# Kernel optimization log

Measured on AMD Instinct MI355X. Metric: run time of the kernel, lower is better.

The kernel has to match this reference:

```python
import jax, jax.numpy as jnp
import numpy as np

HEADS = 16
HEAD_DIM = 64


def _attn(q, k, v):
    # q: [..., Q, h, d], k/v: [..., K, h, d]  (non-causal SDPA, scale 1/sqrt(d))
    scale = 1.0 / np.sqrt(HEAD_DIM).astype(np.float32)
    s = jnp.einsum('...qhd,...khd->...hqk', q, k) * scale
    p = jax.nn.softmax(s, axis=-1)
    return jnp.einsum('...hqk,...khd->...qhd', p, v)


def setup_inputs() -> dict:
    key = jax.random.key(0)
    k0, k1, k2 = jax.random.split(key, 3)
    B, T, H, W, D = 4, 32, 16, 16, 1024
    inner = HEADS * HEAD_DIM
    x = jax.random.normal(k0, (B, T, H, W, D), jnp.float32)
    Wqkv = jax.random.normal(k1, (D, 3 * inner), jnp.float32) / np.sqrt(D)
    Wout = jax.random.normal(k2, (inner, D), jnp.float32) / np.sqrt(inner)
    bout = jnp.zeros((D,), jnp.float32)
    return {"x": x, "Wqkv": Wqkv, "Wout": Wout, "bout": bout, "reference_length": 3}


def reference(x, Wqkv, Wout, bout, reference_length):
    B, T, H, W, D = x.shape
    length = reference_length + 1
    n = T // length            # n_frames (chunks)
    S = H * W                  # tokens per frame
    h, d = HEADS, HEAD_DIM

    qkv = jnp.einsum('bthwD,De->bthwe', x, Wqkv)
    q, k, v = jnp.split(qkv, 3, axis=-1)

    def rs(t):  # -> [B, n, length, S, h, d]
        return t.reshape(B, n, length, S, h, d)

    qr, kr, vr = rs(q), rs(k), rs(v)

    # non-last chunks: query = first frame of chunk, keys/values = remaining r frames
    q_pre = qr[:, :-1, 0]                                             # [B, n-1, S, h, d]
    k_pre = kr[:, :-1, 1:].reshape(B, n - 1, reference_length * S, h, d)
    v_pre = vr[:, :-1, 1:].reshape(B, n - 1, reference_length * S, h, d)
    o_pre = _attn(q_pre, k_pre, v_pre).reshape(B, n - 1, H, W, h * d)

    # last chunk: all `length` frames are queries, keys/values = frames 1..length-1
    q_last = qr[:, -1].reshape(B, length * S, h, d)
    k_last = kr[:, -1, 1:].reshape(B, reference_length * S, h, d)
    v_last = vr[:, -1, 1:].reshape(B, reference_length * S, h, d)
    o_last = _attn(q_last, k_last, v_last).reshape(B, length, H, W, h * d)

    o = jnp.concatenate([o_pre, o_last], axis=1)  # [B, n-1+length, H, W, inner]
    return jnp.einsum('bthwe,eD->bthwD', o, Wout) + bout
```

## Files before the change

### kernel.cpp

```cpp
#include <hip/hip_runtime.h>
#include <hip/hip_bf16.h>

typedef __bf16 bf16;
typedef __bf16 bf16x8 __attribute__((ext_vector_type(8)));
typedef float  f32x4  __attribute__((ext_vector_type(4)));
typedef float  f32x4v __attribute__((ext_vector_type(4)));
typedef unsigned int u32x4 __attribute__((ext_vector_type(4)));
typedef unsigned short u16x4 __attribute__((ext_vector_type(4)));

#define DEV __device__ __forceinline__

DEV void gload_lds16(const bf16* g, bf16* l) {
    __builtin_amdgcn_global_load_lds(
        (__attribute__((address_space(1))) void*)g,
        (__attribute__((address_space(3))) void*)l, 16, 0, 0);
}

DEV bf16x8 as_bf(u32x4 v) { return __builtin_bit_cast(bf16x8, v); }

DEV f32x4 mfma16(bf16x8 a, bf16x8 b, f32x4 c) {
    return __builtin_amdgcn_mfma_f32_16x16x32_bf16(a, b, c, 0, 0, 0);
}

DEV int cvtpk(float lo, float hi) {
    int r;
    asm("v_cvt_pk_bf16_f32 %0, %1, %2" : "=v"(r) : "v"(lo), "v"(hi));
    return r;
}

constexpr int D_   = 1024;
constexpr int S_   = 256;
constexpr int TOUT = 11;
constexpr int MQ   = 4 * TOUT * S_;
constexpr int MKV  = 4 * 8 * 3 * S_;
constexpr int KVL  = 768;

constexpr int PB_WQKV = 768;
constexpr int PB_WOUT = 256;
constexpr int PB_GQ   = MQ  * 128 / 256;
constexpr int PB_GKV  = MKV * 128 / 256;
constexpr int PB_TOT  = PB_WQKV + PB_WOUT + PB_GQ + PB_GKV;

__global__ void prep(const float* __restrict__ x,
                     const float* __restrict__ Wqkv,
                     const float* __restrict__ Wout,
                     bf16* __restrict__ Aq, bf16* __restrict__ Akv,
                     bf16* __restrict__ Wqkv_t, bf16* __restrict__ Wout_t)
{
    __shared__ float T[64][65];
    const int tid = threadIdx.x;
    int wg = blockIdx.x;

    if (wg < PB_WQKV + PB_WOUT) {
        const float* W; bf16* Wt; int N, bid2;
        if (wg < PB_WQKV) { W = Wqkv; Wt = Wqkv_t; N = 3072; bid2 = wg; }
        else              { W = Wout; Wt = Wout_t; N = 1024; bid2 = wg - PB_WQKV; }
        const int kt = bid2 & 15, nt = bid2 >> 4;
        const int k0 = kt * 64, n0 = nt * 64;
        for (int i = 0; i < 16; ++i) {
            const int e = i * 256 + tid;
            const int kk = e >> 6, nn = e & 63;
            T[nn][kk] = W[(size_t)(k0 + kk) * N + n0 + nn];
        }
        __syncthreads();
        for (int i = 0; i < 16; ++i) {
            const int e = i * 256 + tid;
            const int n = e >> 6, kk = e & 63;
            Wt[(size_t)(n0 + n) * 1024 + k0 + kk] = (bf16)T[n][kk];
        }
        return;
    }
    wg -= PB_WQKV + PB_WOUT;

    int row, part;
    const float* src;
    bf16* dst;
    if (wg < PB_GQ) {
        const int idx = wg * 256 + tid;
        row = idx >> 7; part = idx & 127;
        const int b    = row / (TOUT * S_);
        const int r2   = row - b * (TOUT * S_);
        const int tout = r2 >> 8;
        const int s    = r2 & 255;
        const int tx   = tout < 7 ? tout * 4 : 28 + (tout - 7);
        src = x + ((size_t)((b * 32 + tx) * S_ + s)) * D_ + part * 8;
        dst = Aq + (size_t)row * D_ + part * 8;
    } else {
        const int idx = (wg - PB_GQ) * 256 + tid;
        row = idx >> 7; part = idx & 127;
        const int b  = row / 6144;
        const int r2 = row - b * 6144;
        const int c  = r2 / KVL;
        const int j  = r2 - c * KVL;
        const int f  = 1 + (j >> 8);
        const int s  = j & 255;
        const int tx = c * 4 + f;
        src = x + ((size_t)((b * 32 + tx) * S_ + s)) * D_ + part * 8;
        dst = Akv + (size_t)row * D_ + part * 8;
    }
    f32x4v v0 = *(const f32x4v*)src;
    f32x4v v1 = *(const f32x4v*)(src + 4);
    bf16x8 o;
    o[0]=(bf16)v0[0]; o[1]=(bf16)v0[1]; o[2]=(bf16)v0[2]; o[3]=(bf16)v0[3];
    o[4]=(bf16)v1[0]; o[5]=(bf16)v1[1]; o[6]=(bf16)v1[2]; o[7]=(bf16)v1[3];
    *(bf16x8*)dst = o;
}

#define PH_BEGIN() do { \
    __builtin_amdgcn_s_barrier(); \
    asm volatile("s_waitcnt lgkmcnt(0)" ::: "memory"); \
    __builtin_amdgcn_sched_barrier(0); \
    __builtin_amdgcn_s_setprio(1); \
} while(0)

#define PH_MMEND() do { \
    __builtin_amdgcn_s_setprio(0); \
    __builtin_amdgcn_sched_barrier(0); \
} while(0)

#define PH_CLOSE() do { \
    asm volatile("s_waitcnt vmcnt(6)" ::: "memory"); \
    __builtin_amdgcn_s_barrier(); \
} while(0)

#define STAGE_A(bufc, half, tile) do { \
    const bf16* s0_ = pA + (size_t)(half) * 64 * 1024 + (tile) * 64; \
    bf16* d0_ = ldsA + (bufc) * 16384 + (half) * 8192; \
    gload_lds16(s0_, d0_); \
    gload_lds16(s0_ + (size_t)128 * 1024, d0_ + 4096); \
} while(0)

#define STAGE_B(bufc, half, tile) do { \
    const bf16* s0_ = pB + (size_t)(half) * 32 * 1024 + (tile) * 64; \
    bf16* d0_ = ldsB + (bufc) * 16384 + (half) * 8192; \
    gload_lds16(s0_, d0_); \
    gload_lds16(s0_ + (size_t)128 * 1024, d0_ + 4096); \
} while(0)

#define LDAJ(dst, bufc, mh, J) do { \
    const bf16* p_ = sm + (bufc) * 16384 + (mh) * 8192 + (J) * 1024; \
    dst[J][0] = *(const u32x4*)(p_ + eA0); \
    dst[J][1] = *(const u32x4*)(p_ + eA1); \
} while(0)

#define LDBH(dst, bufc, nh) do { \
    const bf16* p_ = sm + 32768 + (bufc) * 16384 + (nh) * 8192; \
    dst[0][0] = *(const u32x4*)(p_ + eB0); \
    dst[0][1] = *(const u32x4*)(p_ + eB1); \
    dst[1][0] = *(const u32x4*)(p_ + 1024 + eB0); \
    dst[1][1] = *(const u32x4*)(p_ + 1024 + eB1); \
} while(0)

#define MMX(av, bv, mh, nh) do { \
    _Pragma("unroll") \
    for (int j_ = 0; j_ < 4; ++j_) { \
        _Pragma("unroll") \
        for (int i_ = 0; i_ < 2; ++i_) { \
            f32x4 c_ = acc[(mh)*4 + j_][(nh)*2 + i_]; \
            c_ = mfma16(as_bf(av[j_][0]), as_bf(bv[i_][0]), c_); \
            c_ = mfma16(as_bf(av[j_][1]), as_bf(bv[i_][1]), c_); \
            acc[(mh)*4 + j_][(nh)*2 + i_] = c_; \
        } \
    } \
} while(0)

#define GEMM_MAINLOOP() do { \
    STAGE_A(0, 0, 0); STAGE_A(0, 1, 0); STAGE_B(0, 0, 0); STAGE_B(0, 1, 0); \
    STAGE_A(1, 0, 1); STAGE_B(1, 0, 1); STAGE_B(1, 1, 1); \
    asm volatile("s_waitcnt vmcnt(6)" ::: "memory"); \
    __builtin_amdgcn_s_barrier(); \
    LDAJ(aX,0,0,0); LDAJ(aX,0,0,1); LDAJ(aX,0,0,2); LDAJ(aX,0,0,3); \
    LDBH(bP,0,0); \
    _Pragma("unroll 1") \
    for (int t = 0; t < 8; ++t) { \
        const int T1 = 2 * t + 1; \
        const int n0 = (2 * t + 2 < 15) ? 2 * t + 2 : 15; \
        const int n1 = (2 * t + 3 < 15) ? 2 * t + 3 : 15; \
        STAGE_A(1, 1, T1); \
        PH_BEGIN(); MMX(aX, bP, 0, 0); PH_MMEND(); \
        LDBH(bQ, 0, 1); LDAJ(aY, 0, 1, 0); \
        PH_CLOSE(); \
        STAGE_A(0, 0, n0); \
        PH_BEGIN(); MMX(aX, bQ, 0, 1); PH_MMEND(); \
        LDAJ(aY, 0, 1, 1); LDAJ(aY, 0, 1, 2); LDAJ(aY, 0, 1, 3); \
        PH_CLOSE(); \
        STAGE_B(0, 0, n0); \
        PH_BEGIN(); MMX(aY, bP, 1, 0); PH_MMEND(); \
        LDAJ(aX, 1, 0, 0); LDAJ(aX, 1, 0, 1); LDAJ(aX, 1, 0, 2); \
        PH_CLOSE(); \
        STAGE_B(0, 1, n0); \
        PH_BEGIN(); MMX(aY, bQ, 1, 1); PH_MMEND(); \
        LDAJ(aX, 1, 0, 3); LDBH(bP, 1, 0); \
        PH_CLOSE(); \
        STAGE_A(0, 1, n0); \
        PH_BEGIN(); MMX(aX, bP, 0, 0); PH_MMEND(); \
        LDBH(bQ, 1, 1); LDAJ(aY, 1, 1, 0); \
        PH_CLOSE(); \
        STAGE_A(1, 0, n1); \
        PH_BEGIN(); MMX(aX, bQ, 0, 1); PH_MMEND(); \
        LDAJ(aY, 1, 1, 1); LDAJ(aY, 1, 1, 2); LDAJ(aY, 1, 1, 3); \
        PH_CLOSE(); \
        STAGE_B(1, 0, n1); \
        PH_BEGIN(); MMX(aY, bP, 1, 0); PH_MMEND(); \
        LDAJ(aX, 0, 0, 0); LDAJ(aX, 0, 0, 1); LDAJ(aX, 0, 0, 2); \
        PH_CLOSE(); \
        STAGE_B(1, 1, n1); \
        PH_BEGIN(); MMX(aY, bQ, 1, 1); PH_MMEND(); \
        LDAJ(aX, 0, 0, 3); LDBH(bP, 0, 0); \
        PH_CLOSE(); \
    } \
    asm volatile("s_waitcnt vmcnt(0) lgkmcnt(0)" ::: "memory"); \
} while(0)

#define GEMM_PREAMBLE() \
    const int wr = wid >> 2, wc = wid & 3; \
    const int l15 = lane & 15, l4 = lane >> 4; \
    const int Rrow = (wid << 3) + (lane >> 3); \
    const int G    = (lane & 7) ^ (lane >> 3); \
    const bf16* pA = A  + (size_t)(bm * 256 + Rrow) * 1024 + G * 8; \
    const int wc1 = Rrow >> 5, cc1 = Rrow & 31; \
    const bf16* pB = Bt + (size_t)(bn * 256 + wc1 * 64 + cc1) * 1024 + G * 8; \
    bf16* ldsA = sm + (wid << 9); \
    bf16* ldsB = sm + 32768 + (wid << 9); \
    const int g0  = l4 ^ (l15 & 7); \
    const int eA0 = wr * 4096 + l15 * 64 + g0 * 8; \
    const int eA1 = eA0 ^ 32; \
    const int eB0 = wc * 2048 + l15 * 64 + g0 * 8; \
    const int eB1 = eB0 ^ 32; \
    f32x4 acc[8][4]; \
    u32x4 aX[4][2], aY[4][2], bP[2][2], bQ[2][2]; \
    { const f32x4 zf_ = {0.f, 0.f, 0.f, 0.f}; \
      _Pragma("unroll") \
      for (int m_ = 0; m_ < 8; ++m_) \
          _Pragma("unroll") \
          for (int n_ = 0; n_ < 4; ++n_) acc[m_][n_] = zf_; }

__global__ __launch_bounds__(512, 2) void gemm_qkv(
    const bf16* __restrict__ Aq, const bf16* __restrict__ Akv,
    const bf16* __restrict__ Wt,
    bf16* __restrict__ Qb, bf16* __restrict__ Kb, bf16* __restrict__ Vt)
{
    __shared__ bf16 sm[65536];
    const int tid = threadIdx.x, lane = tid & 63, wid = tid >> 6;

    int wg = blockIdx.x;
    {
        const int xcd = wg & 7, off = wg >> 3;
        wg = xcd * 118 + off;
    }
    const bool isQ = wg < 176;
    const bf16* A;  const bf16* Bt;  int bm, bn;
    if (isQ) {
        const int sg = wg >> 4, s = wg & 15;
        bm = sg * 4 + (s >> 2);
        bn = s & 3;
        A = Aq;  Bt = Wt;
    } else {
        const int id2 = wg - 176;
        const int sg = id2 >> 4, s = id2 & 15;
        bm = (sg % 24) * 4 + (s >> 2);
        bn = (sg / 24) * 4 + (s & 3);
        A = Akv; Bt = Wt + (size_t)1024 * 1024;
    }

    GEMM_PREAMBLE();
    GEMM_MAINLOOP();

    if (isQ || bn < 4) {
        bf16* C = isQ ? Qb : Kb;
        #pragma unroll
        for (int m = 0; m < 8; ++m) {
            const int row = bm * 256 + wr * 128 + m * 16 + l4 * 4;
            #pragma unroll
            for (int n = 0; n < 4; ++n) {
                const int col = bn * 256 + wc * 64 + n * 16 + l15;
                f32x4 v = acc[m][n];
                #pragma unroll
                for (int r = 0; r < 4; ++r)
                    C[(size_t)(row + r) * 1024 + col] = (bf16)v[r];
            }
        }
    } else {
        const int vb = bm / 3;
        const int j0base = (bm % 3) * 256;
        #pragma unroll
        for (int m = 0; m < 8; ++m) {
            const int j0 = j0base + wr * 128 + m * 16 + l4 * 4;
            #pragma unroll
            for (int n = 0; n < 4; ++n) {
                const int colv = (bn - 4) * 256 + wc * 64 + n * 16 + l15;
                f32x4 v = acc[m][n];
                u16x4 pk;
                #pragma unroll
                for (int r = 0; r < 4; ++r) {
                    bf16 t = (bf16)v[r];
                    pk[r] = __builtin_bit_cast(unsigned short, t);
                }
                *(u16x4*)(Vt + ((size_t)vb * 1024 + colv) * KVL + j0) = pk;
            }
        }
    }
}

__global__ __launch_bounds__(512, 2) void gemm_out(
    const bf16* __restrict__ A, const bf16* __restrict__ Bt,
    float* __restrict__ Cf, const float* __restrict__ bias)
{
    __shared__ bf16 sm[65536];
    const int tid = threadIdx.x, lane = tid & 63, wid = tid >> 6;

    int wg = blockIdx.x;
    {
        const int xcd = wg & 7, off = wg >> 3;
        wg = xcd * 22 + off;
    }
    const int sg = wg >> 4, s = wg & 15;
    const int bm = sg * 4 + (s >> 2), bn = s & 3;

    GEMM_PREAMBLE();
    GEMM_MAINLOOP();

    #pragma unroll
    for (int m = 0; m < 8; ++m) {
        const int row = bm * 256 + wr * 128 + m * 16 + l4 * 4;
        #pragma unroll
        for (int n = 0; n < 4; ++n) {
            const int col = bn * 256 + wc * 64 + n * 16 + l15;
            f32x4 v = acc[m][n];
            const float bs = bias[col];
            #pragma unroll
            for (int r = 0; r < 4; ++r)
                Cf[(size_t)(row + r) * 1024 + col] = v[r] + bs;
        }
    }
}

__global__ __launch_bounds__(256, 4) void attn_fwd(
    const bf16* __restrict__ Q, const bf16* __restrict__ K,
    const bf16* __restrict__ Vt, bf16* __restrict__ O)
{
    __shared__ bf16 Kl[2][2][64][32];
    __shared__ bf16 Vl[2][2][64][32];

    const int tid = threadIdx.x, lane = tid & 63, wid = tid >> 6;
    int bid = blockIdx.x;
    const int h = bid & 15; bid >>= 4;
    const int qt = bid % 44, b = bid / 44;
    const int chunk = qt < 28 ? (qt >> 2) : 7;
    const int qrow0 = b * (TOUT * S_) +
                      (qt < 28 ? chunk * S_ + (qt & 3) * 64 : 7 * S_ + (qt - 28) * 64);

    const bf16* kg = K  + ((size_t)(b * 8 + chunk) * KVL) * 1024 + h * 64;
    const bf16* vg = Vt + ((size_t)((b * 8 + chunk) * 16 + h)) * 64 * KVL;

    const int l15 = lane & 15, l4 = lane >> 4;

    const bf16* qp = Q + (size_t)(qrow0 + wid * 16 + l15) * D_ + h * 64 + l4 * 8;
    u32x4 q0, q1;
    {
        bf16x8 t0 = *(const bf16x8*)qp;
        bf16x8 t1 = *(const bf16x8*)(qp + 32);
        #pragma unroll
        for (int j = 0; j < 8; ++j) {
            t0[j] = (bf16)((float)t0[j] * 0.125f);
            t1[j] = (bf16)((float)t1[j] * 0.125f);
        }
        q0 = __builtin_bit_cast(u32x4, t0);
        q1 = __builtin_bit_cast(u32x4, t1);
    }

    const int R   = wid * 16 + (lane >> 2);
    const int gsw = ((lane & 3) ^ ((lane >> 3) & 3)) * 8;
    const int rg  = (l4 ^ ((l15 >> 1) & 3)) * 8;

    const int baseA = ((2 * (l4 & 1)) * 16 + l15) * 4;
    const int baseB = baseA + 64;
    const bool hi2 = (l4 & 2) != 0;

    float m_s = -1e30f, l_s = 0.f;
    f32x4 oacc[4];
    const f32x4 zf = {0.f, 0.f, 0.f, 0.f};
    #pragma unroll
    for (int m2 = 0; m2 < 4; ++m2) oacc[m2] = zf;

#define ASTAGE(c, t) do { \
    const int kv0_ = (t) * 64; \
    gload_lds16(kg + (size_t)(kv0_ + R) * 1024 + gsw,      &Kl[c][0][0][0] + wid * 512); \
    gload_lds16(kg + (size_t)(kv0_ + R) * 1024 + 32 + gsw, &Kl[c][1][0][0] + wid * 512); \
    gload_lds16(vg + (size_t)R * KVL + kv0_ + gsw,         &Vl[c][0][0][0] + wid * 512); \
    gload_lds16(vg + (size_t)R * KVL + kv0_ + 32 + gsw,    &Vl[c][1][0][0] + wid * 512); \
} while (0)

    ASTAGE(0, 0);
    __syncthreads();

    #pragma unroll 1
    for (int kt = 0; kt < 12; ++kt) {
        const int cur = kt & 1;
        if (kt < 11) ASTAGE(cur ^ 1, kt + 1);

        f32x4 s[4];
        #pragma unroll
        for (int n = 0; n < 4; ++n) {
            const bf16* kp = &Kl[cur][0][n * 16 + l15][0] + rg;
            const u32x4 k0 = *(const u32x4*)kp;
            const u32x4 k1 = *(const u32x4*)(kp + 2048);
            f32x4 t = mfma16(as_bf(k0), as_bf(q0), zf);
            s[n] = mfma16(as_bf(k1), as_bf(q1), t);
        }

        float pm = s[0][0];
        #pragma unroll
        for (int n = 0; n < 4; ++n)
            #pragma unroll
            for (int r = 0; r < 4; ++r) pm = fmaxf(pm, s[n][r]);
        pm = fmaxf(pm, __shfl_xor(pm, 16));
        pm = fmaxf(pm, __shfl_xor(pm, 32));
        const float mn = fmaxf(m_s, pm);
        const float al = __expf(m_s - mn);
        m_s = mn;
        float p[4][4];
        float sum = 0.f;
        #pragma unroll
        for (int n = 0; n < 4; ++n)
            #pragma unroll
            for (int r = 0; r < 4; ++r) {
                const float e = __expf(s[n][r] - mn);
                p[n][r] = e; sum += e;
            }
        sum += __shfl_xor(sum, 16);
        sum += __shfl_xor(sum, 32);
        l_s = l_s * al + sum;
        #pragma unroll
        for (int m2 = 0; m2 < 4; ++m2) oacc[m2] *= al;

        int u[4][2];
        #pragma unroll
        for (int n = 0; n < 4; ++n) {
            u[n][0] = cvtpk(p[n][0], p[n][1]);
            u[n][1] = cvtpk(p[n][2], p[n][3]);
        }

        #pragma unroll
        for (int kk = 0; kk < 2; ++kk) {
            const int e0 = __builtin_amdgcn_ds_bpermute(baseA, u[2 * kk][0]);
            const int f0 = __builtin_amdgcn_ds_bpermute(baseA, u[2 * kk + 1][0]);
            const int e1 = __builtin_amdgcn_ds_bpermute(baseA, u[2 * kk][1]);
            const int f1 = __builtin_amdgcn_ds_bpermute(baseA, u[2 * kk + 1][1]);
            const int e2 = __builtin_amdgcn_ds_bpermute(baseB, u[2 * kk][0]);
            const int f2 = __builtin_amdgcn_ds_bpermute(baseB, u[2 * kk + 1][0]);
            const int e3 = __builtin_amdgcn_ds_bpermute(baseB, u[2 * kk][1]);
            const int f3 = __builtin_amdgcn_ds_bpermute(baseB, u[2 * kk + 1][1]);
            u32x4 pb;
            pb[0] = (unsigned)(hi2 ? f0 : e0);
            pb[1] = (unsigned)(hi2 ? f1 : e1);
            pb[2] = (unsigned)(hi2 ? f2 : e2);
            pb[3] = (unsigned)(hi2 ? f3 : e3);
            #pragma unroll
            for (int m2 = 0; m2 < 4; ++m2) {
                const u32x4 vf = *(const u32x4*)(&Vl[cur][kk][m2 * 16 + l15][0] + rg);
                oacc[m2] = mfma16(as_bf(vf), as_bf(pb), oacc[m2]);
            }
        }
        __syncthreads();
    }
#undef ASTAGE

    const float inv = 1.f / l_s;
    bf16* sc = &Kl[0][0][0][0] + wid * 1152;
    #pragma unroll
    for (int m2 = 0; m2 < 4; ++m2)
        #pragma unroll
        for (int r = 0; r < 4; ++r)
            sc[l15 * 72 + m2 * 16 + l4 * 4 + r] = (bf16)(oacc[m2][r] * inv);
    const int rq = lane >> 2, rd = (lane & 3) * 16;
    const bf16* sr = sc + rq * 72 + rd;
    const u32x4 o0 = *(const u32x4*)sr;
    const u32x4 o1 = *(const u32x4*)(sr + 8);
    bf16* op = O + (size_t)(qrow0 + wid * 16 + rq) * D_ + h * 64 + rd;
    *(u32x4*)op = o0;
    *(u32x4*)(op + 8) = o1;
}

extern "C" void kernel_launch(void* const* d_in, const int* in_sizes, int n_in,
                              void* d_out, int out_size, void* d_ws, size_t ws_size,
                              hipStream_t stream) {
    (void)in_sizes; (void)n_in; (void)out_size; (void)ws_size;
    const float* x    = (const float*)d_in[0];
    const float* Wqkv = (const float*)d_in[1];
    const float* Wout = (const float*)d_in[2];
    const float* bout = (const float*)d_in[3];

    bf16* Aq     = (bf16*)d_ws;
    bf16* Akv    = Aq     + (size_t)MQ  * 1024;
    bf16* Wqkv_t = Akv    + (size_t)MKV * 1024;
    bf16* Wout_t = Wqkv_t + (size_t)3072 * 1024;
    bf16* Qb     = Wout_t + (size_t)1024 * 1024;
    bf16* Kb     = Qb     + (size_t)MQ  * 1024;
    bf16* Vtb    = Kb     + (size_t)MKV * 1024;
    bf16* Ob     = Aq;

    prep<<<PB_TOT, 256, 0, stream>>>(x, Wqkv, Wout, Aq, Akv, Wqkv_t, Wout_t);

    gemm_qkv<<<944, 512, 0, stream>>>(Aq, Akv, Wqkv_t, Qb, Kb, Vtb);

    attn_fwd<<<4 * 44 * 16, 256, 0, stream>>>(Qb, Kb, Vtb, Ob);

    gemm_out<<<176, 512, 0, stream>>>(Ob, Wout_t, (float*)d_out, bout);
}
```

Measured before the change: 284.5 us.

## Restructure GEMM mainloop into four phases with double B fragment registers

The 8-phase-per-iteration GEMM main loop becomes 4 phases, each issuing two MMX blocks and two stage loads, with B fragments double-buffered (bP0/bQ0/bP1/bQ1) and the wait lowered to vmcnt(4). The aim is to halve the number of barriers and waitcnt stalls per K tile and give each phase more MFMA work to hide LDS and global latency. The cost is higher register pressure from the extra B fragments under launch_bounds(512,2), and the prologue now waits on vmcnt(0).

```diff
diff --git a/kernel.cpp b/kernel.cpp
--- a/kernel.cpp
+++ b/kernel.cpp
@@ -118,8 +118,8 @@
     __builtin_amdgcn_sched_barrier(0); \
 } while(0)
 
-#define PH_CLOSE() do { \
-    asm volatile("s_waitcnt vmcnt(6)" ::: "memory"); \
+#define PH_CLOSE4() do { \
+    asm volatile("s_waitcnt vmcnt(4)" ::: "memory"); \
     __builtin_amdgcn_s_barrier(); \
 } while(0)
 
@@ -167,47 +167,35 @@
 #define GEMM_MAINLOOP() do { \
     STAGE_A(0, 0, 0); STAGE_A(0, 1, 0); STAGE_B(0, 0, 0); STAGE_B(0, 1, 0); \
     STAGE_A(1, 0, 1); STAGE_B(1, 0, 1); STAGE_B(1, 1, 1); \
-    asm volatile("s_waitcnt vmcnt(6)" ::: "memory"); \
+    asm volatile("s_waitcnt vmcnt(0)" ::: "memory"); \
     __builtin_amdgcn_s_barrier(); \
     LDAJ(aX,0,0,0); LDAJ(aX,0,0,1); LDAJ(aX,0,0,2); LDAJ(aX,0,0,3); \
-    LDBH(bP,0,0); \
+    LDBH(bP0,0,0); LDBH(bQ0,0,1); \
     _Pragma("unroll 1") \
     for (int t = 0; t < 8; ++t) { \
         const int T1 = 2 * t + 1; \
         const int n0 = (2 * t + 2 < 15) ? 2 * t + 2 : 15; \
         const int n1 = (2 * t + 3 < 15) ? 2 * t + 3 : 15; \
-        STAGE_A(1, 1, T1); \
-        PH_BEGIN(); MMX(aX, bP, 0, 0); PH_MMEND(); \
-        LDBH(bQ, 0, 1); LDAJ(aY, 0, 1, 0); \
-        PH_CLOSE(); \
-        STAGE_A(0, 0, n0); \
-        PH_BEGIN(); MMX(aX, bQ, 0, 1); PH_MMEND(); \
-        LDAJ(aY, 0, 1, 1); LDAJ(aY, 0, 1, 2); LDAJ(aY, 0, 1, 3); \
-        PH_CLOSE(); \
-        STAGE_B(0, 0, n0); \
-        PH_BEGIN(); MMX(aY, bP, 1, 0); PH_MMEND(); \
-        LDAJ(aX, 1, 0, 0); LDAJ(aX, 1, 0, 1); LDAJ(aX, 1, 0, 2); \
-        PH_CLOSE(); \
-        STAGE_B(0, 1, n0); \
-        PH_BEGIN(); MMX(aY, bQ, 1, 1); PH_MMEND(); \
-        LDAJ(aX, 1, 0, 3); LDBH(bP, 1, 0); \
-        PH_CLOSE(); \
-        STAGE_A(0, 1, n0); \
-        PH_BEGIN(); MMX(aX, bP, 0, 0); PH_MMEND(); \
-        LDBH(bQ, 1, 1); LDAJ(aY, 1, 1, 0); \
-        PH_CLOSE(); \
-        STAGE_A(1, 0, n1); \
-        PH_BEGIN(); MMX(aX, bQ, 0, 1); PH_MMEND(); \
-        LDAJ(aY, 1, 1, 1); LDAJ(aY, 1, 1, 2); LDAJ(aY, 1, 1, 3); \
-        PH_CLOSE(); \
-        STAGE_B(1, 0, n1); \
-        PH_BEGIN(); MMX(aY, bP, 1, 0); PH_MMEND(); \
-        LDAJ(aX, 0, 0, 0); LDAJ(aX, 0, 0, 1); LDAJ(aX, 0, 0, 2); \
-        PH_CLOSE(); \
-        STAGE_B(1, 1, n1); \
-        PH_BEGIN(); MMX(aY, bQ, 1, 1); PH_MMEND(); \
-        LDAJ(aX, 0, 0, 3); LDBH(bP, 0, 0); \
-        PH_CLOSE(); \
+        STAGE_A(1, 1, T1); STAGE_B(0, 0, n0); \
+        PH_BEGIN(); MMX(aX, bP0, 0, 0); MMX(aX, bQ0, 0, 1); PH_MMEND(); \
+        LDAJ(aY, 0, 1, 0); LDAJ(aY, 0, 1, 1); LDAJ(aY, 0, 1, 2); LDAJ(aY, 0, 1, 3); \
+        LDBH(bP1, 1, 0); \
+        PH_CLOSE4(); \
+        STAGE_A(0, 0, n0); STAGE_B(0, 1, n0); \
+        PH_BEGIN(); MMX(aY, bP0, 1, 0); MMX(aY, bQ0, 1, 1); PH_MMEND(); \
+        LDAJ(aX, 1, 0, 0); LDAJ(aX, 1, 0, 1); LDAJ(aX, 1, 0, 2); LDAJ(aX, 1, 0, 3); \
+        LDBH(bQ1, 1, 1); \
+        PH_CLOSE4(); \
+        STAGE_A(0, 1, n0); STAGE_B(1, 0, n1); \
+        PH_BEGIN(); MMX(aX, bP1, 0, 0); MMX(aX, bQ1, 0, 1); PH_MMEND(); \
+        LDAJ(aY, 1, 1, 0); LDAJ(aY, 1, 1, 1); LDAJ(aY, 1, 1, 2); LDAJ(aY, 1, 1, 3); \
+        LDBH(bP0, 0, 0); \
+        PH_CLOSE4(); \
+        STAGE_A(1, 0, n1); STAGE_B(1, 1, n1); \
+        PH_BEGIN(); MMX(aY, bP1, 1, 0); MMX(aY, bQ1, 1, 1); PH_MMEND(); \
+        LDAJ(aX, 0, 0, 0); LDAJ(aX, 0, 0, 1); LDAJ(aX, 0, 0, 2); LDAJ(aX, 0, 0, 3); \
+        LDBH(bQ0, 0, 1); \
+        PH_CLOSE4(); \
     } \
     asm volatile("s_waitcnt vmcnt(0) lgkmcnt(0)" ::: "memory"); \
 } while(0)
@@ -228,7 +216,7 @@
     const int eB0 = wc * 2048 + l15 * 64 + g0 * 8; \
     const int eB1 = eB0 ^ 32; \
     f32x4 acc[8][4]; \
-    u32x4 aX[4][2], aY[4][2], bP[2][2], bQ[2][2]; \
+    u32x4 aX[4][2], aY[4][2], bP0[2][2], bQ0[2][2], bP1[2][2], bQ1[2][2]; \
     { const f32x4 zf_ = {0.f, 0.f, 0.f, 0.f}; \
       _Pragma("unroll") \
       for (int m_ = 0; m_ < 8; ++m_) \
```

After: 285.1 us. Within noise of the previous version (+0.2%).

## Process four query tiles per wave in attention to reuse K/V LDS loads

Applied to the files above, without the earlier changes.

Each attention block now covers 256 query rows instead of 64, with every wave handling four 16-row query groups against the same K/V tiles held in registers. K and V fragments are read from LDS once per tile and reused across the four groups. This cuts global K/V traffic and LDS reads per query fourfold, but register pressure rises (launch bounds drop to 2 blocks per SM) and the grid shrinks to 704 blocks, which may leave some compute units underused. The epilogue reuses the LDS scratch, alternating two slots per wave across the groups.

```diff
diff --git a/kernel.cpp b/kernel.cpp
--- a/kernel.cpp
+++ b/kernel.cpp
@@ -335,7 +335,7 @@
     }
 }
 
-__global__ __launch_bounds__(256, 4) void attn_fwd(
+__global__ __launch_bounds__(256, 2) void attn_fwd(
     const bf16* __restrict__ Q, const bf16* __restrict__ K,
     const bf16* __restrict__ Vt, bf16* __restrict__ O)
 {
@@ -345,19 +345,19 @@
     const int tid = threadIdx.x, lane = tid & 63, wid = tid >> 6;
     int bid = blockIdx.x;
     const int h = bid & 15; bid >>= 4;
-    const int qt = bid % 44, b = bid / 44;
-    const int chunk = qt < 28 ? (qt >> 2) : 7;
-    const int qrow0 = b * (TOUT * S_) +
-                      (qt < 28 ? chunk * S_ + (qt & 3) * 64 : 7 * S_ + (qt - 28) * 64);
+    const int cb = bid % 11, b = bid / 11;
+    const int chunk = cb < 7 ? cb : 7;
+    const int qrow0 = b * (TOUT * S_) + cb * 256 + wid * 64;
 
     const bf16* kg = K  + ((size_t)(b * 8 + chunk) * KVL) * 1024 + h * 64;
     const bf16* vg = Vt + ((size_t)((b * 8 + chunk) * 16 + h)) * 64 * KVL;
 
     const int l15 = lane & 15, l4 = lane >> 4;
 
-    const bf16* qp = Q + (size_t)(qrow0 + wid * 16 + l15) * D_ + h * 64 + l4 * 8;
-    u32x4 q0, q1;
-    {
+    u32x4 qg[4][2];
+    #pragma unroll
+    for (int g = 0; g < 4; ++g) {
+        const bf16* qp = Q + (size_t)(qrow0 + g * 16 + l15) * D_ + h * 64 + l4 * 8;
         bf16x8 t0 = *(const bf16x8*)qp;
         bf16x8 t1 = *(const bf16x8*)(qp + 32);
         #pragma unroll
@@ -365,8 +365,8 @@
             t0[j] = (bf16)((float)t0[j] * 0.125f);
             t1[j] = (bf16)((float)t1[j] * 0.125f);
         }
-        q0 = __builtin_bit_cast(u32x4, t0);
-        q1 = __builtin_bit_cast(u32x4, t1);
+        qg[g][0] = __builtin_bit_cast(u32x4, t0);
+        qg[g][1] = __builtin_bit_cast(u32x4, t1);
     }
 
     const int R   = wid * 16 + (lane >> 2);
@@ -377,11 +377,15 @@
     const int baseB = baseA + 64;
     const bool hi2 = (l4 & 2) != 0;
 
-    float m_s = -1e30f, l_s = 0.f;
-    f32x4 oacc[4];
+    float m_s[4], l_s[4];
+    f32x4 oacc[4][4];
     const f32x4 zf = {0.f, 0.f, 0.f, 0.f};
     #pragma unroll
-    for (int m2 = 0; m2 < 4; ++m2) oacc[m2] = zf;
+    for (int g = 0; g < 4; ++g) {
+        m_s[g] = -1e30f; l_s[g] = 0.f;
+        #pragma unroll
+        for (int m2 = 0; m2 < 4; ++m2) oacc[g][m2] = zf;
+    }
 
 #define ASTAGE(c, t) do { \
     const int kv0_ = (t) * 64; \
@@ -399,87 +403,103 @@
         const int cur = kt & 1;
         if (kt < 11) ASTAGE(cur ^ 1, kt + 1);
 
-        f32x4 s[4];
+        u32x4 kv[8];
         #pragma unroll
         for (int n = 0; n < 4; ++n) {
             const bf16* kp = &Kl[cur][0][n * 16 + l15][0] + rg;
-            const u32x4 k0 = *(const u32x4*)kp;
-            const u32x4 k1 = *(const u32x4*)(kp + 2048);
-            f32x4 t = mfma16(as_bf(k0), as_bf(q0), zf);
-            s[n] = mfma16(as_bf(k1), as_bf(q1), t);
-        }
-
-        float pm = s[0][0];
-        #pragma unroll
-        for (int n = 0; n < 4; ++n)
-            #pragma unroll
-            for (int r = 0; r < 4; ++r) pm = fmaxf(pm, s[n][r]);
-        pm = fmaxf(pm, __shfl_xor(pm, 16));
-        pm = fmaxf(pm, __shfl_xor(pm, 32));
-        const float mn = fmaxf(m_s, pm);
-        const float al = __expf(m_s - mn);
-        m_s = mn;
-        float p[4][4];
-        float sum = 0.f;
-        #pragma unroll
-        for (int n = 0; n < 4; ++n)
-            #pragma unroll
-            for (int r = 0; r < 4; ++r) {
-                const float e = __expf(s[n][r] - mn);
-                p[n][r] = e; sum += e;
+            kv[n * 2]     = *(const u32x4*)kp;
+            kv[n * 2 + 1] = *(const u32x4*)(kp + 2048);
+        }
+
+        int u[4][4][2];
+        #pragma unroll
+        for (int g = 0; g < 4; ++g) {
+            f32x4 s[4];
+            #pragma unroll
+            for (int n = 0; n < 4; ++n) {
+                f32x4 t = mfma16(as_bf(kv[n * 2]), as_bf(qg[g][0]), zf);
+                s[n] = mfma16(as_bf(kv[n * 2 + 1]), as_bf(qg[g][1]), t);
             }
-        sum += __shfl_xor(sum, 16);
-        sum += __shfl_xor(sum, 32);
-        l_s = l_s * al + sum;
-        #pragma unroll
-        for (int m2 = 0; m2 < 4; ++m2) oacc[m2] *= al;
-
-        int u[4][2];
-        #pragma unroll
-        for (int n = 0; n < 4; ++n) {
-            u[n][0] = cvtpk(p[n][0], p[n][1]);
-            u[n][1] = cvtpk(p[n][2], p[n][3]);
-        }
+            float pm = s[0][0];
+            #pragma unroll
+            for (int n = 0; n < 4; ++n)
+                #pragma unroll
+                for (int r = 0; r < 4; ++r) pm = fmaxf(pm, s[n][r]);
+            pm = fmaxf(pm, __shfl_xor(pm, 16));
+            pm = fmaxf(pm, __shfl_xor(pm, 32));
+            const float mn = fmaxf(m_s[g], pm);
+            const float al = __expf(m_s[g] - mn);
+            m_s[g] = mn;
+            float p[4][4];
+            float sum = 0.f;
+            #pragma unroll
+            for (int n = 0; n < 4; ++n)
+                #pragma unroll
+                for (int r = 0; r < 4; ++r) {
+                    const float e = __expf(s[n][r] - mn);
+                    p[n][r] = e; sum += e;
+                }
+            sum += __shfl_xor(sum, 16);
+            sum += __shfl_xor(sum, 32);
+            l_s[g] = l_s[g] * al + sum;
+            #pragma unroll
+            for (int m2 = 0; m2 < 4; ++m2) oacc[g][m2] *= al;
+            #pragma unroll
+            for (int n = 0; n < 4; ++n) {
+                u[g][n][0] = cvtpk(p[n][0], p[n][1]);
+                u[g][n][1] = cvtpk(p[n][2], p[n][3]);
+            }
+        }
+
+        #pragma unroll
+        for (int kk = 0; kk < 2; ++kk)
+            #pragma unroll
+            for (int m2 = 0; m2 < 4; ++m2)
+                kv[kk * 4 + m2] = *(const u32x4*)(&Vl[cur][kk][m2 * 16 + l15][0] + rg);
 
         #pragma unroll
         for (int kk = 0; kk < 2; ++kk) {
-            const int e0 = __builtin_amdgcn_ds_bpermute(baseA, u[2 * kk][0]);
-            const int f0 = __builtin_amdgcn_ds_bpermute(baseA, u[2 * kk + 1][0]);
-            const int e1 = __builtin_amdgcn_ds_bpermute(baseA, u[2 * kk][1]);
-            const int f1 = __builtin_amdgcn_ds_bpermute(baseA, u[2 * kk + 1][1]);
-            const int e2 = __builtin_amdgcn_ds_bpermute(baseB, u[2 * kk][0]);
-            const int f2 = __builtin_amdgcn_ds_bpermute(baseB, u[2 * kk + 1][0]);
-            const int e3 = __builtin_amdgcn_ds_bpermute(baseB, u[2 * kk][1]);
-            const int f3 = __builtin_amdgcn_ds_bpermute(baseB, u[2 * kk + 1][1]);
-            u32x4 pb;
-            pb[0] = (unsigned)(hi2 ? f0 : e0);
-            pb[1] = (unsigned)(hi2 ? f1 : e1);
-            pb[2] = (unsigned)(hi2 ? f2 : e2);
-            pb[3] = (unsigned)(hi2 ? f3 : e3);
-            #pragma unroll
-            for (int m2 = 0; m2 < 4; ++m2) {
-                const u32x4 vf = *(const u32x4*)(&Vl[cur][kk][m2 * 16 + l15][0] + rg);
-                oacc[m2] = mfma16(as_bf(vf), as_bf(pb), oacc[m2]);
+            #pragma unroll
+            for (int g = 0; g < 4; ++g) {
+                const int e0 = __builtin_amdgcn_ds_bpermute(baseA, u[g][2 * kk][0]);
+                const int f0 = __builtin_amdgcn_ds_bpermute(baseA, u[g][2 * kk + 1][0]);
+                const int e1 = __builtin_amdgcn_ds_bpermute(baseA, u[g][2 * kk][1]);
+                const int f1 = __builtin_amdgcn_ds_bpermute(baseA, u[g][2 * kk + 1][1]);
+                const int e2 = __builtin_amdgcn_ds_bpermute(baseB, u[g][2 * kk][0]);
+                const int f2 = __builtin_amdgcn_ds_bpermute(baseB, u[g][2 * kk + 1][0]);
+                const int e3 = __builtin_amdgcn_ds_bpermute(baseB, u[g][2 * kk][1]);
+                const int f3 = __builtin_amdgcn_ds_bpermute(baseB, u[g][2 * kk + 1][1]);
+                u32x4 pb;
+                pb[0] = (unsigned)(hi2 ? f0 : e0);
+                pb[1] = (unsigned)(hi2 ? f1 : e1);
+                pb[2] = (unsigned)(hi2 ? f2 : e2);
+                pb[3] = (unsigned)(hi2 ? f3 : e3);
+                #pragma unroll
+                for (int m2 = 0; m2 < 4; ++m2)
+                    oacc[g][m2] = mfma16(as_bf(kv[kk * 4 + m2]), as_bf(pb), oacc[g][m2]);
             }
         }
         __syncthreads();
     }
 #undef ASTAGE
 
-    const float inv = 1.f / l_s;
-    bf16* sc = &Kl[0][0][0][0] + wid * 1152;
     #pragma unroll
-    for (int m2 = 0; m2 < 4; ++m2)
-        #pragma unroll
-        for (int r = 0; r < 4; ++r)
-            sc[l15 * 72 + m2 * 16 + l4 * 4 + r] = (bf16)(oacc[m2][r] * inv);
-    const int rq = lane >> 2, rd = (lane & 3) * 16;
-    const bf16* sr = sc + rq * 72 + rd;
-    const u32x4 o0 = *(const u32x4*)sr;
-    const u32x4 o1 = *(const u32x4*)(sr + 8);
-    bf16* op = O + (size_t)(qrow0 + wid * 16 + rq) * D_ + h * 64 + rd;
-    *(u32x4*)op = o0;
-    *(u32x4*)(op + 8) = o1;
+    for (int g = 0; g < 4; ++g) {
+        const float inv = 1.f / l_s[g];
+        bf16* sc = &Kl[0][0][0][0] + (wid * 2 + (g & 1)) * 1152;
+        #pragma unroll
+        for (int m2 = 0; m2 < 4; ++m2)
+            #pragma unroll
+            for (int r = 0; r < 4; ++r)
+                sc[l15 * 72 + m2 * 16 + l4 * 4 + r] = (bf16)(oacc[g][m2][r] * inv);
+        const int rq = lane >> 2, rd = (lane & 3) * 16;
+        const bf16* sr = sc + rq * 72 + rd;
+        const u32x4 o0 = *(const u32x4*)sr;
+        const u32x4 o1 = *(const u32x4*)(sr + 8);
+        bf16* op = O + (size_t)(qrow0 + g * 16 + rq) * D_ + h * 64 + rd;
+        *(u32x4*)op = o0;
+        *(u32x4*)(op + 8) = o1;
+    }
 }
 
 extern "C" void kernel_launch(void* const* d_in, const int* in_sizes, int n_in,
@@ -504,7 +524,7 @@
 
     gemm_qkv<<<944, 512, 0, stream>>>(Aq, Akv, Wqkv_t, Qb, Kb, Vtb);
 
-    attn_fwd<<<4 * 44 * 16, 256, 0, stream>>>(Qb, Kb, Vtb, Ob);
+    attn_fwd<<<4 * 11 * 16, 256, 0, stream>>>(Qb, Kb, Vtb, Ob);
 
     gemm_out<<<176, 512, 0, stream>>>(Ob, Wout_t, (float*)d_out, bout);
 }
```

New measurement: 285.0 us. No clear change (+0.2%).
